# Performance work log

Measured on AMD Instinct MI355X. Metric: run time of the kernel, lower is better.

## Reference

```python
import math
import jax, jax.numpy as jnp
import numpy as np

N = 20000
E = 640000
H = 256          # hidden_channels
HEADS = 8
HD = H // HEADS  # head_dim = 32
RBF = 64
CUT = 5.0
EPS = 1e-5


def setup_inputs() -> dict:
    key = jax.random.key(0)
    ks = jax.random.split(key, 24)
    g = lambda k, shape, scale: (jax.random.normal(k, shape, dtype=jnp.float32) * scale)
    inp = {
        "x": jax.random.normal(ks[0], (N, H), dtype=jnp.float32),
        "vec": jax.random.normal(ks[1], (N, 3, H), dtype=jnp.float32),
        "edge_index": jax.random.randint(ks[2], (2, E), 0, N),
        "r_ij": jax.random.uniform(ks[3], (E,), dtype=jnp.float32) * CUT,
        "f_ij": jax.random.normal(ks[4], (E, RBF), dtype=jnp.float32),
        "d_ij": jax.random.normal(ks[5], (E, 3), dtype=jnp.float32),
        # parameters (weights stored as [in, out], applied as x @ W + b)
        "ln_w": jnp.ones((H,), jnp.float32),
        "ln_b": jnp.zeros((H,), jnp.float32),
        "Wq": g(ks[6], (H, H), 1.0 / math.sqrt(H)),
        "bq": jnp.zeros((H,), jnp.float32),
        "Wk": g(ks[7], (H, H), 1.0 / math.sqrt(H)),
        "bk": jnp.zeros((H,), jnp.float32),
        "Wv": g(ks[8], (H, 3 * H), 1.0 / math.sqrt(H)),
        "bv": jnp.zeros((3 * H,), jnp.float32),
        "Wo": g(ks[9], (H, 3 * H), 1.0 / math.sqrt(H)),
        "bo": jnp.zeros((3 * H,), jnp.float32),
        "Wvec": g(ks[10], (H, 3 * H), 1.0 / math.sqrt(H)),  # no bias
        "Wdk": g(ks[11], (RBF, H), 1.0 / math.sqrt(RBF)),
        "bdk": jnp.zeros((H,), jnp.float32),
        "Wdv": g(ks[12], (RBF, 3 * H), 1.0 / math.sqrt(RBF)),
        "bdv": jnp.zeros((3 * H,), jnp.float32),
    }
    return inp


def reference(x, vec, edge_index, r_ij, f_ij, d_ij,
              ln_w, ln_b, Wq, bq, Wk, bk, Wv, bv, Wo, bo,
              Wvec, Wdk, bdk, Wdv, bdv):
    silu = jax.nn.silu
    n = x.shape[0]

    # LayerNorm over hidden dim
    mu = x.mean(-1, keepdims=True)
    var = ((x - mu) ** 2).mean(-1, keepdims=True)
    xn = (x - mu) / jnp.sqrt(var + EPS) * ln_w + ln_b

    q = (xn @ Wq + bq).reshape(n, HEADS, HD)
    k = (xn @ Wk + bk).reshape(n, HEADS, HD)
    v = (xn @ Wv + bv).reshape(n, HEADS, 3 * HD)

    # vec_proj: [N,3,H] @ [H,3H] -> split into three [N,3,H]
    vec1, vec2, vec3 = jnp.split(vec @ Wvec, 3, axis=-1)
    vec_dot = (vec1 * vec2).sum(axis=1)              # [N, H]
    vec_h = vec.reshape(n, 3, HEADS, HD)

    dk = silu(f_ij @ Wdk + bdk).reshape(-1, HEADS, HD)        # [E,h,hd]
    dv = silu(f_ij @ Wdv + bdv).reshape(-1, HEADS, 3 * HD)    # [E,h,3hd]

    src = edge_index[0]  # j (source)
    dst = edge_index[1]  # i (target), aggregation index

    # per-edge attention with cosine cutoff (cutoff_lower = 0)
    attn = (q[dst] * k[src] * dk).sum(-1)                      # [E, h]
    cut = 0.5 * (jnp.cos(r_ij * (math.pi / CUT)) + 1.0)
    cut = cut * (r_ij < CUT).astype(cut.dtype)
    attn = silu(attn) * cut[:, None]

    v_j = v[src] * dv                                          # [E,h,3hd]
    xm, v1m, v2m = jnp.split(v_j, 3, axis=2)                   # each [E,h,hd]
    xm = xm * attn[..., None]                                  # [E,h,hd]
    # [E,3,h,hd]
    vecm = vec_h[src] * v1m[:, None] + v2m[:, None] * d_ij[:, :, None, None]

    x_agg = jax.ops.segment_sum(xm, dst, num_segments=n).reshape(n, H)
    vec_agg = jax.ops.segment_sum(vecm, dst, num_segments=n).reshape(n, 3, H)

    o1, o2, o3 = jnp.split(x_agg @ Wo + bo, 3, axis=1)
    dx = vec_dot * o2 + o3
    dvec = vec3 * o1[:, None] + vec_agg
    return dx, dvec
```

## Files before the change

### kernel.cpp

```cpp
#include <hip/hip_runtime.h>

#define NN 20000
#define EE 640000
#define H 256
#define H3 768

typedef __attribute__((ext_vector_type(8))) short bfrag;
typedef __attribute__((ext_vector_type(4))) float f32x4;
typedef __attribute__((ext_vector_type(2))) unsigned short u16x2;
typedef __attribute__((ext_vector_type(4))) unsigned short u16x4;
typedef unsigned short u16;

__device__ __forceinline__ float silu_f(float x){ return x / (1.f + __expf(-x)); }

__device__ __forceinline__ u16 f2bf(float f){
  union { float fv; unsigned u; } a; a.fv = f;
  unsigned r = a.u + 0x7fffu + ((a.u >> 16) & 1u);
  return (u16)(r >> 16);
}
__device__ __forceinline__ float bf2f(u16 u){
  union { unsigned u32; float f; } a; a.u32 = ((unsigned)u) << 16; return a.f;
}

__global__ __launch_bounds__(256) void ln_kernel(
    const float* __restrict__ x, const float* __restrict__ w,
    const float* __restrict__ b, u16* __restrict__ xnh, u16* __restrict__ xnl)
{
  int n = blockIdx.x, t = threadIdx.x;
  float v = x[(size_t)n*H + t];
  float s1 = v, s2 = v*v;
  #pragma unroll
  for(int o=32;o>0;o>>=1){ s1 += __shfl_down(s1,o,64); s2 += __shfl_down(s2,o,64); }
  __shared__ float r1[4], r2[4];
  if((t&63)==0){ r1[t>>6]=s1; r2[t>>6]=s2; }
  __syncthreads();
  float mu  = (r1[0]+r1[1]+r1[2]+r1[3]) * (1.f/256.f);
  float ex2 = (r2[0]+r2[1]+r2[2]+r2[3]) * (1.f/256.f);
  float inv = rsqrtf(ex2 - mu*mu + 1e-5f);
  float y = (v - mu)*inv*w[t] + b[t];
  u16 h = f2bf(y);
  xnh[(size_t)n*H + t] = h;
  xnl[(size_t)n*H + t] = f2bf(y - bf2f(h));
}

__global__ __launch_bounds__(256) void wconv(
    const float* __restrict__ W, int ldw,
    u16* __restrict__ oh, u16* __restrict__ ol, int mode)
{
  int idx = blockIdx.x*256 + threadIdx.x;
  int n = idx >> 8, k = idx & 255;
  int c = n;
  if(mode == 1){
    int y = n >> 7, j = n & 127;
    c = (j < 64) ? (y*64 + j) : (256 + y*64 + (j - 64));
  }
  float f = W[(size_t)k*ldw + c];
  u16 h = f2bf(f);
  oh[idx] = h;
  ol[idx] = f2bf(f - bf2f(h));
}

__global__ __launch_bounds__(256) void cvt_vec(
    const float* __restrict__ src, u16* __restrict__ hi, u16* __restrict__ lo, int n4)
{
  int i = blockIdx.x*256 + threadIdx.x;
  if(i < n4){
    float4 v = ((const float4*)src)[i];
    u16x4 oh, olo;
    float a[4] = {v.x, v.y, v.z, v.w};
    #pragma unroll
    for(int j=0;j<4;j++){
      u16 h = f2bf(a[j]);
      oh[j]  = h;
      olo[j] = f2bf(a[j] - bf2f(h));
    }
    ((u16x4*)hi)[i] = oh;
    ((u16x4*)lo)[i] = olo;
  }
}

template<int OUT>
__global__ __launch_bounds__(256) void gemm_split(
    const u16* __restrict__ Ah, const u16* __restrict__ Al,
    const u16* __restrict__ Bh, const u16* __restrict__ Bl,
    const float* __restrict__ bias,
    float* __restrict__ Cf, u16* __restrict__ Ch, int ldw, int M)
{
  int tid  = threadIdx.x;
  int wid  = tid >> 6, lane = tid & 63;
  int ln15 = lane & 15, quad = lane >> 4;
  int wr = wid >> 1, wc = wid & 1;
  int m0 = blockIdx.x*128 + wr*64;
  int n0 = blockIdx.y*128 + wc*64;

  int arow[4];
  #pragma unroll
  for(int mi=0;mi<4;mi++){
    int r = m0 + mi*16 + ln15;
    arow[mi] = (r < M) ? r : (M-1);
  }
  int ncol[4];
  #pragma unroll
  for(int ni=0;ni<4;ni++) ncol[ni] = n0 + ni*16 + ln15;

  f32x4 acc[4][4] = {};

  #pragma unroll 2
  for(int ks=0; ks<8; ks++){
    int kb = ks*32 + quad*8;
    bfrag ah[4], al[4], bh[4], bl[4];
    #pragma unroll
    for(int mi=0;mi<4;mi++){
      ah[mi] = *(const bfrag*)(Ah + ((size_t)arow[mi] << 8) + kb);
      al[mi] = *(const bfrag*)(Al + ((size_t)arow[mi] << 8) + kb);
    }
    #pragma unroll
    for(int ni=0;ni<4;ni++){
      bh[ni] = *(const bfrag*)(Bh + ((size_t)ncol[ni] << 8) + kb);
      bl[ni] = *(const bfrag*)(Bl + ((size_t)ncol[ni] << 8) + kb);
    }
    #pragma unroll
    for(int mi=0;mi<4;mi++)
      #pragma unroll
      for(int ni=0;ni<4;ni++){
        acc[mi][ni] = __builtin_amdgcn_mfma_f32_16x16x32_bf16(ah[mi], bh[ni], acc[mi][ni], 0,0,0);
        acc[mi][ni] = __builtin_amdgcn_mfma_f32_16x16x32_bf16(ah[mi], bl[ni], acc[mi][ni], 0,0,0);
        acc[mi][ni] = __builtin_amdgcn_mfma_f32_16x16x32_bf16(al[mi], bh[ni], acc[mi][ni], 0,0,0);
      }
  }

  #pragma unroll
  for(int mi=0;mi<4;mi++){
    #pragma unroll
    for(int ni=0;ni<4;ni++){
      int col = ncol[ni];
      float bs = bias ? bias[col] : 0.f;
      #pragma unroll
      for(int r=0;r<4;r++){
        int row = m0 + mi*16 + quad*4 + r;
        if(row < M){
          float v = acc[mi][ni][r] + bs;
          if(OUT == 0) Cf[(size_t)row*ldw + col] = v;
          else         Ch[(size_t)row*ldw + col] = f2bf(v);
        }
      }
    }
  }
}

__global__ __launch_bounds__(256) void gemm_vecdot(
    const u16* __restrict__ Ah, const u16* __restrict__ Al,
    const u16* __restrict__ Bh, const u16* __restrict__ Bl,
    float* __restrict__ vd)
{
  __shared__ float l1[96][66];
  __shared__ float l2[96][66];
  int tid  = threadIdx.x;
  int wid  = tid >> 6, lane = tid & 63;
  int ln15 = lane & 15, quad = lane >> 4;
  int wr = wid >> 1, wc = wid & 1;
  int m0 = blockIdx.x*96;
  int y  = blockIdx.y;
  int rowb = wr*48;

  int arow[3];
  #pragma unroll
  for(int mi=0;mi<3;mi++) arow[mi] = m0 + rowb + mi*16 + ln15;
  int ncol[4];
  #pragma unroll
  for(int ni=0;ni<4;ni++) ncol[ni] = y*128 + wc*64 + ni*16 + ln15;

  f32x4 acc[3][4] = {};

  #pragma unroll 2
  for(int ks=0; ks<8; ks++){
    int kb = ks*32 + quad*8;
    bfrag ah[3], al[3], bh[4], bl[4];
    #pragma unroll
    for(int mi=0;mi<3;mi++){
      ah[mi] = *(const bfrag*)(Ah + ((size_t)arow[mi] << 8) + kb);
      al[mi] = *(const bfrag*)(Al + ((size_t)arow[mi] << 8) + kb);
    }
    #pragma unroll
    for(int ni=0;ni<4;ni++){
      bh[ni] = *(const bfrag*)(Bh + ((size_t)ncol[ni] << 8) + kb);
      bl[ni] = *(const bfrag*)(Bl + ((size_t)ncol[ni] << 8) + kb);
    }
    #pragma unroll
    for(int mi=0;mi<3;mi++)
      #pragma unroll
      for(int ni=0;ni<4;ni++){
        acc[mi][ni] = __builtin_amdgcn_mfma_f32_16x16x32_bf16(ah[mi], bh[ni], acc[mi][ni], 0,0,0);
        acc[mi][ni] = __builtin_amdgcn_mfma_f32_16x16x32_bf16(ah[mi], bl[ni], acc[mi][ni], 0,0,0);
        acc[mi][ni] = __builtin_amdgcn_mfma_f32_16x16x32_bf16(al[mi], bh[ni], acc[mi][ni], 0,0,0);
      }
  }

  #pragma unroll
  for(int mi=0;mi<3;mi++)
    #pragma unroll
    for(int ni=0;ni<4;ni++)
      #pragma unroll
      for(int r=0;r<4;r++){
        int lr = rowb + mi*16 + quad*4 + r;
        int lc = ni*16 + ln15;
        if(wc == 0) l1[lr][lc] = acc[mi][ni][r];
        else        l2[lr][lc] = acc[mi][ni][r];
      }
  __syncthreads();

  #pragma unroll
  for(int i=0;i<8;i++){
    int id  = i*256 + tid;
    int n_l = id >> 6, c = id & 63;
    float s = 0.f;
    #pragma unroll
    for(int d=0;d<3;d++) s += l1[n_l*3+d][c] * l2[n_l*3+d][c];
    vd[((size_t)(blockIdx.x*32 + n_l) << 8) + y*64 + c] = s;
  }
}

__global__ __launch_bounds__(256) void hist_kernel(const int* __restrict__ ei, int* __restrict__ deg){
  int e = blockIdx.x*256 + threadIdx.x;
  if(e < EE) atomicAdd(&deg[ei[EE + e]], 1);
}

__global__ __launch_bounds__(1024) void scan_kernel(const int* __restrict__ deg, int* __restrict__ offs){
  __shared__ int ps[1024];
  int t = threadIdx.x;
  int base = t*20;
  int s = 0;
  for(int i=0;i<20;i++){ int idx = base+i; if(idx < NN) s += deg[idx]; }
  ps[t] = s; __syncthreads();
  for(int off=1; off<1024; off<<=1){
    int v = (t>=off) ? ps[t-off] : 0;
    __syncthreads();
    ps[t] += v;
    __syncthreads();
  }
  int run = (t==0) ? 0 : ps[t-1];
  for(int i=0;i<20;i++){
    int idx = base+i;
    if(idx <= NN){
      offs[idx] = run;
      if(idx < NN) run += deg[idx];
    }
  }
}

__global__ __launch_bounds__(256) void scatter_kernel(
    const int* __restrict__ ei, const int* __restrict__ offs,
    int* __restrict__ cursor, int* __restrict__ perm)
{
  int e = blockIdx.x*256 + threadIdx.x;
  if(e >= EE) return;
  int d = ei[EE + e];
  int r = atomicAdd(&cursor[d], 1);
  perm[offs[d] + r] = e;
}

__global__ __launch_bounds__(256) void conv_wdk(const float* __restrict__ Wdk, short* __restrict__ wdkf){
  int idx = blockIdx.x*256 + threadIdx.x;
  int k = idx >> 8, c = idx & 255;
  int g = c >> 6, rem = c & 63, n15 = rem >> 2, p = rem & 3;
  int half = k >> 5, quad = (k >> 3) & 3, j = k & 7;
  wdkf[(g*4+p)*1024 + half*512 + quad*128 + n15*8 + j] = (short)f2bf(Wdk[k*H + c]);
}

__global__ __launch_bounds__(256) void conv_wdv(const float* __restrict__ Wdv, short* __restrict__ wdvf){
  int idx = blockIdx.x*256 + threadIdx.x;
  int k = idx / 768, c = idx % 768;
  int h = c / 96, jj = c % 96;
  int st = jj >> 5, r32 = jj & 31, n15 = r32 >> 1, p = r32 & 1;
  int sub = h*6 + st*2 + p;
  int half = k >> 5, quad = (k >> 3) & 3, j = k & 7;
  wdvf[sub*1024 + half*512 + quad*128 + n15*8 + j] = (short)f2bf(Wdv[k*H3 + c]);
}

__global__ __launch_bounds__(256,3) void edge_kernel(
    const int* __restrict__ ei, const float* __restrict__ rij,
    const float* __restrict__ fij, const float* __restrict__ dij,
    const float* __restrict__ qg, const u16* __restrict__ kh,
    const u16* __restrict__ vh, const u16* __restrict__ vech,
    const short* __restrict__ wdkf, const short* __restrict__ wdvf,
    const float* __restrict__ bdk, const float* __restrict__ bdv,
    const int* __restrict__ offs, const int* __restrict__ perm,
    u16* __restrict__ xaggh, u16* __restrict__ xaggl, float* __restrict__ dvec)
{
  __shared__ float accs_x[4][256];
  __shared__ float accs_v[4][768];
  __shared__ float attn_s[4][16][8];
  __shared__ int   esrc_s[4][16];
  __shared__ float ecut_s[4][16];
  __shared__ float emask_s[4][16];
  __shared__ float edij_s[4][3][16];

  int tid  = threadIdx.x;
  int wv   = tid >> 6, lane = tid & 63;
  int ln15 = lane & 15, quad = lane >> 4;
  int n    = blockIdx.x*4 + wv;
  int rs = offs[n], re = offs[n+1];

  #pragma unroll
  for(int i=0;i<4;i++)  accs_x[wv][i*64 + lane] = 0.f;
  #pragma unroll
  for(int i=0;i<12;i++) accs_v[wv][i*64 + lane] = 0.f;

  float qreg[16], bkreg[16];
  #pragma unroll
  for(int g=0; g<4; g++){
    float4 t = *(const float4*)(qg + (size_t)n*H + g*64 + 4*ln15);
    qreg[g*4+0]=t.x; qreg[g*4+1]=t.y; qreg[g*4+2]=t.z; qreg[g*4+3]=t.w;
    float4 u = *(const float4*)(bdk + g*64 + 4*ln15);
    bkreg[g*4+0]=u.x; bkreg[g*4+1]=u.y; bkreg[g*4+2]=u.z; bkreg[g*4+3]=u.w;
  }

  for(int base = rs; base < re; base += 16){
    int idx = base + ln15;
    bool val = idx < re;
    int e = perm[val ? idx : rs];
    if(quad == 0){
      esrc_s[wv][ln15] = ei[e];
      float r = rij[e];
      float cu = 0.5f*(__cosf(r*0.6283185307f)+1.f);
      cu = (r < 5.f) ? cu : 0.f;
      ecut_s[wv][ln15]  = val ? cu : 0.f;
      emask_s[wv][ln15] = val ? 1.f : 0.f;
      edij_s[wv][0][ln15] = dij[e*3+0];
      edij_s[wv][1][ln15] = dij[e*3+1];
      edij_s[wv][2][ln15] = dij[e*3+2];
    }
    bfrag af0, af1;
    {
      const float* fr = fij + (size_t)e*64 + quad*8;
      float4 fa = *(const float4*)fr;
      float4 fb = *(const float4*)(fr+4);
      float4 fc = *(const float4*)(fr+32);
      float4 fd = *(const float4*)(fr+36);
      af0[0]=(short)f2bf(fa.x); af0[1]=(short)f2bf(fa.y); af0[2]=(short)f2bf(fa.z); af0[3]=(short)f2bf(fa.w);
      af0[4]=(short)f2bf(fb.x); af0[5]=(short)f2bf(fb.y); af0[6]=(short)f2bf(fb.z); af0[7]=(short)f2bf(fb.w);
      af1[0]=(short)f2bf(fc.x); af1[1]=(short)f2bf(fc.y); af1[2]=(short)f2bf(fc.z); af1[3]=(short)f2bf(fc.w);
      af1[4]=(short)f2bf(fd.x); af1[5]=(short)f2bf(fd.y); af1[6]=(short)f2bf(fd.z); af1[7]=(short)f2bf(fd.w);
    }
    int sns[4]; float mk[4];
    #pragma unroll
    for(int r=0;r<4;r++){
      int el = quad*4 + r;
      sns[r] = esrc_s[wv][el];
      mk[r]  = emask_s[wv][el];
    }

    u16x4 kr[4][4];
    #pragma unroll
    for(int g=0;g<4;g++)
      #pragma unroll
      for(int r=0;r<4;r++)
        kr[g][r] = *(const u16x4*)(kh + (size_t)sns[r]*H + g*64 + 4*ln15);

    #pragma unroll
    for(int g=0;g<4;g++){
      float lgg[4] = {0.f,0.f,0.f,0.f};
      #pragma unroll
      for(int p=0;p<4;p++){
        const short* wp = wdkf + (g*4+p)*1024 + quad*128 + ln15*8;
        bfrag b0 = *(const bfrag*)wp;
        bfrag b1 = *(const bfrag*)(wp + 512);
        f32x4 acc = {0.f,0.f,0.f,0.f};
        acc = __builtin_amdgcn_mfma_f32_16x16x32_bf16(af0, b0, acc, 0,0,0);
        acc = __builtin_amdgcn_mfma_f32_16x16x32_bf16(af1, b1, acc, 0,0,0);
        float bias = bkreg[g*4+p], qv = qreg[g*4+p];
        #pragma unroll
        for(int r=0;r<4;r++){
          float dk = silu_f(acc[r] + bias);
          lgg[r] += dk * qv * bf2f(kr[g][r][p]);
        }
      }
      #pragma unroll
      for(int r=0;r<4;r++){
        lgg[r] += __shfl_xor(lgg[r],1,64);
        lgg[r] += __shfl_xor(lgg[r],2,64);
        lgg[r] += __shfl_xor(lgg[r],4,64);
      }
      if((ln15 & 7) == 0){
        int hh = 2*g + (ln15 >> 3);
        #pragma unroll
        for(int r=0;r<4;r++){
          int el = quad*4 + r;
          attn_s[wv][el][hh] = silu_f(lgg[r]) * ecut_s[wv][el];
        }
      }
    }

    #pragma unroll 1
    for(int h=0;h<8;h++){
      u16x2 vld[3][4], vcl[3][4];
      #pragma unroll
      for(int st=0;st<3;st++)
        #pragma unroll
        for(int r=0;r<4;r++)
          vld[st][r] = *(const u16x2*)(vh + (size_t)sns[r]*H3 + h*96 + st*32 + 2*ln15);
      #pragma unroll
      for(int d=0;d<3;d++)
        #pragma unroll
        for(int r=0;r<4;r++)
          vcl[d][r] = *(const u16x2*)(vech + (size_t)sns[r]*H3 + d*H + h*32 + 2*ln15);
      float bb[6];
      #pragma unroll
      for(int st=0;st<3;st++){
        float2 b2 = *(const float2*)(bdv + h*96 + st*32 + 2*ln15);
        bb[st*2] = b2.x; bb[st*2+1] = b2.y;
      }
      float at[4];
      #pragma unroll
      for(int r=0;r<4;r++) at[r] = attn_s[wv][quad*4+r][h];

      float v1v[2][4], vjv[2][4];
      float xmt[2] = {0.f, 0.f};
      #pragma unroll
      for(int st=0;st<3;st++){
        #pragma unroll
        for(int p=0;p<2;p++){
          const short* wp = wdvf + (h*6+st*2+p)*1024 + quad*128 + ln15*8;
          bfrag b0 = *(const bfrag*)wp;
          bfrag b1 = *(const bfrag*)(wp + 512);
          f32x4 acc = {0.f,0.f,0.f,0.f};
          acc = __builtin_amdgcn_mfma_f32_16x16x32_bf16(af0, b0, acc, 0,0,0);
          acc = __builtin_amdgcn_mfma_f32_16x16x32_bf16(af1, b1, acc, 0,0,0);
          float bias = bb[st*2+p];
          #pragma unroll
          for(int r=0;r<4;r++){
            float dvv = silu_f(acc[r] + bias) * mk[r];
            float vj = bf2f(vld[st][r][p]) * dvv;
            if(st == 0)      xmt[p]    += vj * at[r];
            else if(st == 1) v1v[p][r]  = vj;
            else             vjv[p][r]  = vj;
          }
        }
      }
      #pragma unroll
      for(int p=0;p<2;p++){
        xmt[p] += __shfl_xor(xmt[p],16,64);
        xmt[p] += __shfl_xor(xmt[p],32,64);
      }
      if(quad == 0){
        accs_x[wv][h*32 + 2*ln15 + 0] += xmt[0];
        accs_x[wv][h*32 + 2*ln15 + 1] += xmt[1];
      }
      #pragma unroll
      for(int d=0;d<3;d++){
        float t0 = 0.f, t1 = 0.f;
        #pragma unroll
        for(int r=0;r<4;r++){
          float dj = edij_s[wv][d][quad*4+r];
          t0 += bf2f(vcl[d][r][0]) * v1v[0][r] + dj * vjv[0][r];
          t1 += bf2f(vcl[d][r][1]) * v1v[1][r] + dj * vjv[1][r];
        }
        t0 += __shfl_xor(t0,16,64); t0 += __shfl_xor(t0,32,64);
        t1 += __shfl_xor(t1,16,64); t1 += __shfl_xor(t1,32,64);
        if(quad == 0){
          accs_v[wv][d*H + h*32 + 2*ln15 + 0] += t0;
          accs_v[wv][d*H + h*32 + 2*ln15 + 1] += t1;
        }
      }
    }
  }

  #pragma unroll
  for(int j=0;j<4;j++){
    float v = accs_x[wv][j*64 + lane];
    u16 h = f2bf(v);
    xaggh[(size_t)n*H + j*64 + lane] = h;
    xaggl[(size_t)n*H + j*64 + lane] = f2bf(v - bf2f(h));
  }
  #pragma unroll
  for(int j=0;j<12;j++) dvec[(size_t)n*H3 + j*64 + lane] = accs_v[wv][j*64 + lane];
}

__global__ __launch_bounds__(256) void final_kernel(
    const float* __restrict__ ob, const float* __restrict__ vd,
    const float* __restrict__ vp3, float* __restrict__ out)
{
  int i = blockIdx.x*256 + threadIdx.x;
  int n = i >> 8, c = i & 255;
  float o1 = ob[(size_t)n*H3 + c];
  float o2 = ob[(size_t)n*H3 + 256 + c];
  float o3 = ob[(size_t)n*H3 + 512 + c];
  out[i] = vd[i]*o2 + o3;
  float* dvec = out + (size_t)NN*H;
  #pragma unroll
  for(int d=0;d<3;d++){
    dvec[(size_t)n*H3 + d*H + c] += vp3[(size_t)(3*n+d)*256 + c] * o1;
  }
}

extern "C" void kernel_launch(void* const* d_in, const int* in_sizes, int n_in,
                              void* d_out, int out_size, void* d_ws, size_t ws_size,
                              hipStream_t stream){
  (void)in_sizes; (void)n_in; (void)out_size; (void)ws_size;
  const float* x    = (const float*)d_in[0];
  const float* vec  = (const float*)d_in[1];
  const int*   ei   = (const int*)d_in[2];
  const float* rij  = (const float*)d_in[3];
  const float* fij  = (const float*)d_in[4];
  const float* dij  = (const float*)d_in[5];
  const float* ln_w = (const float*)d_in[6];
  const float* ln_b = (const float*)d_in[7];
  const float* Wq   = (const float*)d_in[8];
  const float* bq   = (const float*)d_in[9];
  const float* Wk   = (const float*)d_in[10];
  const float* bk   = (const float*)d_in[11];
  const float* Wv   = (const float*)d_in[12];
  const float* bv   = (const float*)d_in[13];
  const float* Wo   = (const float*)d_in[14];
  const float* bo   = (const float*)d_in[15];
  const float* Wvec = (const float*)d_in[16];
  const float* Wdk  = (const float*)d_in[17];
  const float* bdk  = (const float*)d_in[18];
  const float* Wdv  = (const float*)d_in[19];
  const float* bdv  = (const float*)d_in[20];
  float* out = (float*)d_out;
  float* ws  = (float*)d_ws;

  float* vd    = ws;
  float* ob    = ws +  5120000;
  float* vp3   = ws + 20480000;
  float* qb    = ws + 35840000;
  u16*   kh    = (u16*)(ws + 40960000);
  u16*   vh    = (u16*)(ws + 43520000);
  u16*   vech  = (u16*)(ws + 51200000);
  u16*   vecl  = (u16*)(ws + 58880000);
  u16*   xnh   = (u16*)(ws + 66560000);
  u16*   xnl   = (u16*)(ws + 69120000);
  u16*   xaggh = (u16*)(ws + 71680000);
  u16*   xaggl = (u16*)(ws + 74240000);
  u16*   wt    = (u16*)(ws + 76800000);
  int*   deg    = (int*)(ws + 77530000);
  int*   offs   = deg + 20032;
  int*   cursor = offs + 20032;
  int*   perm   = cursor + 20032;
  short* wdkf   = (short*)(perm + 640000);
  short* wdvf   = wdkf + 16384;

  u16* wtq_h = wt;            u16* wtq_l = wt +   65536;
  u16* wtk_h = wt +  131072;  u16* wtk_l = wt +  196608;
  u16* wtv_h = wt +  262144;  u16* wtv_l = wt +  458752;
  u16* wto_h = wt +  655360;  u16* wto_l = wt +  851968;
  u16* wtp_h = wt + 1048576;  u16* wtp_l = wt + 1179648;
  u16* wt3_h = wt + 1310720;  u16* wt3_l = wt + 1376256;

  float* dvec = out + (size_t)NN*H;

  ln_kernel<<<20000, 256, 0, stream>>>(x, ln_w, ln_b, xnh, xnl);

  wconv<<<256, 256, 0, stream>>>(Wq,        256, wtq_h, wtq_l, 0);
  wconv<<<256, 256, 0, stream>>>(Wk,        256, wtk_h, wtk_l, 0);
  wconv<<<768, 256, 0, stream>>>(Wv,        768, wtv_h, wtv_l, 0);
  wconv<<<768, 256, 0, stream>>>(Wo,        768, wto_h, wto_l, 0);
  wconv<<<512, 256, 0, stream>>>(Wvec,      768, wtp_h, wtp_l, 1);
  wconv<<<256, 256, 0, stream>>>(Wvec + 512,768, wt3_h, wt3_l, 0);

  gemm_split<0><<<dim3(157,2), 256, 0, stream>>>(xnh, xnl, wtq_h, wtq_l, bq, qb, nullptr, 256, 20000);
  gemm_split<1><<<dim3(157,2), 256, 0, stream>>>(xnh, xnl, wtk_h, wtk_l, bk, nullptr, kh, 256, 20000);
  gemm_split<1><<<dim3(157,6), 256, 0, stream>>>(xnh, xnl, wtv_h, wtv_l, bv, nullptr, vh, 768, 20000);

  cvt_vec<<<15000, 256, 0, stream>>>(vec, vech, vecl, 3840000);
  gemm_vecdot<<<dim3(625,4), 256, 0, stream>>>(vech, vecl, wtp_h, wtp_l, vd);
  gemm_split<0><<<dim3(469,2), 256, 0, stream>>>(vech, vecl, wt3_h, wt3_l, nullptr, vp3, nullptr, 256, 60000);

  hipMemsetAsync(deg,    0, 20000*sizeof(int), stream);
  hipMemsetAsync(cursor, 0, 20000*sizeof(int), stream);
  hist_kernel<<<2500, 256, 0, stream>>>(ei, deg);
  scan_kernel<<<1, 1024, 0, stream>>>(deg, offs);
  scatter_kernel<<<2500, 256, 0, stream>>>(ei, offs, cursor, perm);
  conv_wdk<<<64,  256, 0, stream>>>(Wdk, wdkf);
  conv_wdv<<<192, 256, 0, stream>>>(Wdv, wdvf);

  edge_kernel<<<5000, 256, 0, stream>>>(ei, rij, fij, dij, qb, kh, vh, vech,
                                        wdkf, wdvf, bdk, bdv, offs, perm,
                                        xaggh, xaggl, dvec);

  gemm_split<0><<<dim3(157,6), 256, 0, stream>>>(xaggh, xaggl, wto_h, wto_l, bo, ob, nullptr, 768, 20000);
  final_kernel<<<20000, 256, 0, stream>>>(ob, vd, vp3, out);
}
```

Measured before the change: 2.100 ms.

## Merge weight prep kernels, fuse K and V GEMMs, raise edge kernel occupancy

```diff
diff --git a/kernel.cpp b/kernel.cpp
--- a/kernel.cpp
+++ b/kernel.cpp
@@ -43,11 +43,11 @@
   xnl[(size_t)n*H + t] = f2bf(y - bf2f(h));
 }
 
-__global__ __launch_bounds__(256) void wconv(
+__device__ __forceinline__ void wconv_body(
     const float* __restrict__ W, int ldw,
-    u16* __restrict__ oh, u16* __restrict__ ol, int mode)
-{
-  int idx = blockIdx.x*256 + threadIdx.x;
+    u16* __restrict__ oh, u16* __restrict__ ol, int mode, int bidx)
+{
+  int idx = bidx*256 + threadIdx.x;
   int n = idx >> 8, k = idx & 255;
   int c = n;
   if(mode == 1){
@@ -58,6 +58,60 @@
   u16 h = f2bf(f);
   oh[idx] = h;
   ol[idx] = f2bf(f - bf2f(h));
+}
+
+__device__ __forceinline__ void convdk_body(
+    const float* __restrict__ Wdk, short* __restrict__ wdkf, int bidx)
+{
+  int idx = bidx*256 + threadIdx.x;
+  int k = idx >> 8, c = idx & 255;
+  int g = c >> 6, rem = c & 63, n15 = rem >> 2, p = rem & 3;
+  int half = k >> 5, quad = (k >> 3) & 3, j = k & 7;
+  wdkf[(g*4+p)*1024 + half*512 + quad*128 + n15*8 + j] = (short)f2bf(Wdk[k*H + c]);
+}
+
+__device__ __forceinline__ void convdv_body(
+    const float* __restrict__ Wdv, short* __restrict__ wdvf, int bidx)
+{
+  int idx = bidx*256 + threadIdx.x;
+  int k = idx / 768, c = idx % 768;
+  int h = c / 96, jj = c % 96;
+  int st = jj >> 5, r32 = jj & 31, n15 = r32 >> 1, p = r32 & 1;
+  int sub = h*6 + st*2 + p;
+  int half = k >> 5, quad = (k >> 3) & 3, j = k & 7;
+  wdvf[sub*1024 + half*512 + quad*128 + n15*8 + j] = (short)f2bf(Wdv[k*H3 + c]);
+}
+
+__global__ __launch_bounds__(256) void prep_kernel(
+    const float* __restrict__ Wq, const float* __restrict__ Wk,
+    const float* __restrict__ Wv, const float* __restrict__ Wo,
+    const float* __restrict__ Wvec,
+    const float* __restrict__ Wdk, const float* __restrict__ Wdv,
+    const float* __restrict__ bk, const float* __restrict__ bv,
+    u16* __restrict__ wtq_h, u16* __restrict__ wtq_l,
+    u16* __restrict__ wtkv_h, u16* __restrict__ wtkv_l,
+    u16* __restrict__ wto_h, u16* __restrict__ wto_l,
+    u16* __restrict__ wtp_h, u16* __restrict__ wtp_l,
+    u16* __restrict__ wt3_h, u16* __restrict__ wt3_l,
+    short* __restrict__ wdkf, short* __restrict__ wdvf,
+    float* __restrict__ bkv, int* __restrict__ deg, int* __restrict__ cursor)
+{
+  int bx = blockIdx.x;
+  if(bx < 256){        wconv_body(Wq,       256, wtq_h,          wtq_l,          0, bx); }
+  else if(bx < 512){   wconv_body(Wk,       256, wtkv_h,         wtkv_l,         0, bx-256); }
+  else if(bx < 1280){  wconv_body(Wv,       768, wtkv_h+65536,   wtkv_l+65536,   0, bx-512); }
+  else if(bx < 2048){  wconv_body(Wo,       768, wto_h,          wto_l,          0, bx-1280); }
+  else if(bx < 2560){  wconv_body(Wvec,     768, wtp_h,          wtp_l,          1, bx-2048); }
+  else if(bx < 2816){  wconv_body(Wvec+512, 768, wt3_h,          wt3_l,          0, bx-2560); }
+  else if(bx < 2880){  convdk_body(Wdk, wdkf, bx-2816); }
+  else if(bx < 3072){  convdv_body(Wdv, wdvf, bx-2880); }
+  else if(bx < 3076){
+    int i = (bx-3072)*256 + threadIdx.x;
+    bkv[i] = (i < 256) ? bk[i] : bv[i-256];
+  } else {
+    int i = (bx-3076)*256 + threadIdx.x;
+    if(i < NN){ deg[i] = 0; cursor[i] = 0; }
+  }
 }
 
 __global__ __launch_bounds__(256) void cvt_vec(
@@ -259,29 +313,11 @@
   perm[offs[d] + r] = e;
 }
 
-__global__ __launch_bounds__(256) void conv_wdk(const float* __restrict__ Wdk, short* __restrict__ wdkf){
-  int idx = blockIdx.x*256 + threadIdx.x;
-  int k = idx >> 8, c = idx & 255;
-  int g = c >> 6, rem = c & 63, n15 = rem >> 2, p = rem & 3;
-  int half = k >> 5, quad = (k >> 3) & 3, j = k & 7;
-  wdkf[(g*4+p)*1024 + half*512 + quad*128 + n15*8 + j] = (short)f2bf(Wdk[k*H + c]);
-}
-
-__global__ __launch_bounds__(256) void conv_wdv(const float* __restrict__ Wdv, short* __restrict__ wdvf){
-  int idx = blockIdx.x*256 + threadIdx.x;
-  int k = idx / 768, c = idx % 768;
-  int h = c / 96, jj = c % 96;
-  int st = jj >> 5, r32 = jj & 31, n15 = r32 >> 1, p = r32 & 1;
-  int sub = h*6 + st*2 + p;
-  int half = k >> 5, quad = (k >> 3) & 3, j = k & 7;
-  wdvf[sub*1024 + half*512 + quad*128 + n15*8 + j] = (short)f2bf(Wdv[k*H3 + c]);
-}
-
-__global__ __launch_bounds__(256,3) void edge_kernel(
+__global__ __launch_bounds__(256,4) void edge_kernel(
     const int* __restrict__ ei, const float* __restrict__ rij,
     const float* __restrict__ fij, const float* __restrict__ dij,
-    const float* __restrict__ qg, const u16* __restrict__ kh,
-    const u16* __restrict__ vh, const u16* __restrict__ vech,
+    const float* __restrict__ qg, const u16* __restrict__ kvh,
+    const u16* __restrict__ vech,
     const short* __restrict__ wdkf, const short* __restrict__ wdvf,
     const float* __restrict__ bdk, const float* __restrict__ bdv,
     const int* __restrict__ offs, const int* __restrict__ perm,
@@ -355,7 +391,7 @@
     for(int g=0;g<4;g++)
       #pragma unroll
       for(int r=0;r<4;r++)
-        kr[g][r] = *(const u16x4*)(kh + (size_t)sns[r]*H + g*64 + 4*ln15);
+        kr[g][r] = *(const u16x4*)(kvh + ((size_t)sns[r] << 10) + g*64 + 4*ln15);
 
     #pragma unroll
     for(int g=0;g<4;g++){
@@ -398,7 +434,7 @@
       for(int st=0;st<3;st++)
         #pragma unroll
         for(int r=0;r<4;r++)
-          vld[st][r] = *(const u16x2*)(vh + (size_t)sns[r]*H3 + h*96 + st*32 + 2*ln15);
+          vld[st][r] = *(const u16x2*)(kvh + ((size_t)sns[r] << 10) + 256 + h*96 + st*32 + 2*ln15);
       #pragma unroll
       for(int d=0;d<3;d++)
         #pragma unroll
@@ -525,8 +561,7 @@
   float* ob    = ws +  5120000;
   float* vp3   = ws + 20480000;
   float* qb    = ws + 35840000;
-  u16*   kh    = (u16*)(ws + 40960000);
-  u16*   vh    = (u16*)(ws + 43520000);
+  u16*   kvh   = (u16*)(ws + 40960000);
   u16*   vech  = (u16*)(ws + 51200000);
   u16*   vecl  = (u16*)(ws + 58880000);
   u16*   xnh   = (u16*)(ws + 66560000);
@@ -534,6 +569,7 @@
   u16*   xaggh = (u16*)(ws + 71680000);
   u16*   xaggl = (u16*)(ws + 74240000);
   u16*   wt    = (u16*)(ws + 76800000);
+  float* bkv   = ws + 77522000;
   int*   deg    = (int*)(ws + 77530000);
   int*   offs   = deg + 20032;
   int*   cursor = offs + 20032;
@@ -541,41 +577,33 @@
   short* wdkf   = (short*)(perm + 640000);
   short* wdvf   = wdkf + 16384;
 
-  u16* wtq_h = wt;            u16* wtq_l = wt +   65536;
-  u16* wtk_h = wt +  131072;  u16* wtk_l = wt +  196608;
-  u16* wtv_h = wt +  262144;  u16* wtv_l = wt +  458752;
-  u16* wto_h = wt +  655360;  u16* wto_l = wt +  851968;
-  u16* wtp_h = wt + 1048576;  u16* wtp_l = wt + 1179648;
-  u16* wt3_h = wt + 1310720;  u16* wt3_l = wt + 1376256;
+  u16* wtq_h  = wt;            u16* wtq_l  = wt +   65536;
+  u16* wtkv_h = wt +  131072;  u16* wtkv_l = wt +  393216;
+  u16* wto_h  = wt +  655360;  u16* wto_l  = wt +  851968;
+  u16* wtp_h  = wt + 1048576;  u16* wtp_l  = wt + 1179648;
+  u16* wt3_h  = wt + 1310720;  u16* wt3_l  = wt + 1376256;
 
   float* dvec = out + (size_t)NN*H;
 
+  prep_kernel<<<3155, 256, 0, stream>>>(Wq, Wk, Wv, Wo, Wvec, Wdk, Wdv, bk, bv,
+                                        wtq_h, wtq_l, wtkv_h, wtkv_l, wto_h, wto_l,
+                                        wtp_h, wtp_l, wt3_h, wt3_l,
+                                        wdkf, wdvf, bkv, deg, cursor);
+
   ln_kernel<<<20000, 256, 0, stream>>>(x, ln_w, ln_b, xnh, xnl);
 
-  wconv<<<256, 256, 0, stream>>>(Wq,        256, wtq_h, wtq_l, 0);
-  wconv<<<256, 256, 0, stream>>>(Wk,        256, wtk_h, wtk_l, 0);
-  wconv<<<768, 256, 0, stream>>>(Wv,        768, wtv_h, wtv_l, 0);
-  wconv<<<768, 256, 0, stream>>>(Wo,        768, wto_h, wto_l, 0);
-  wconv<<<512, 256, 0, stream>>>(Wvec,      768, wtp_h, wtp_l, 1);
-  wconv<<<256, 256, 0, stream>>>(Wvec + 512,768, wt3_h, wt3_l, 0);
-
-  gemm_split<0><<<dim3(157,2), 256, 0, stream>>>(xnh, xnl, wtq_h, wtq_l, bq, qb, nullptr, 256, 20000);
-  gemm_split<1><<<dim3(157,2), 256, 0, stream>>>(xnh, xnl, wtk_h, wtk_l, bk, nullptr, kh, 256, 20000);
-  gemm_split<1><<<dim3(157,6), 256, 0, stream>>>(xnh, xnl, wtv_h, wtv_l, bv, nullptr, vh, 768, 20000);
+  gemm_split<0><<<dim3(157,2), 256, 0, stream>>>(xnh, xnl, wtq_h,  wtq_l,  bq,  qb, nullptr, 256,  20000);
+  gemm_split<1><<<dim3(157,8), 256, 0, stream>>>(xnh, xnl, wtkv_h, wtkv_l, bkv, nullptr, kvh, 1024, 20000);
 
   cvt_vec<<<15000, 256, 0, stream>>>(vec, vech, vecl, 3840000);
   gemm_vecdot<<<dim3(625,4), 256, 0, stream>>>(vech, vecl, wtp_h, wtp_l, vd);
   gemm_split<0><<<dim3(469,2), 256, 0, stream>>>(vech, vecl, wt3_h, wt3_l, nullptr, vp3, nullptr, 256, 60000);
 
-  hipMemsetAsync(deg,    0, 20000*sizeof(int), stream);
-  hipMemsetAsync(cursor, 0, 20000*sizeof(int), stream);
   hist_kernel<<<2500, 256, 0, stream>>>(ei, deg);
   scan_kernel<<<1, 1024, 0, stream>>>(deg, offs);
   scatter_kernel<<<2500, 256, 0, stream>>>(ei, offs, cursor, perm);
-  conv_wdk<<<64,  256, 0, stream>>>(Wdk, wdkf);
-  conv_wdv<<<192, 256, 0, stream>>>(Wdv, wdvf);
-
-  edge_kernel<<<5000, 256, 0, stream>>>(ei, rij, fij, dij, qb, kh, vh, vech,
+
+  edge_kernel<<<5000, 256, 0, stream>>>(ei, rij, fij, dij, qb, kvh, vech,
                                         wdkf, wdvf, bdk, bdv, offs, perm,
                                         xaggh, xaggl, dvec);
 
```

New measurement: 2.319 ms. 10.4% more time.
